# Kernel optimization log

Hardware: AMD Instinct MI355X
Metric: run time of the kernel (lower is better)

The kernel has to match this reference:

```python
import jax, jax.numpy as jnp
import numpy as np


def setup_inputs() -> dict:
    key = jax.random.key(0)
    k1, k2 = jax.random.split(key)
    B = 16384
    y_pred = jax.random.normal(k1, (B,), dtype=jnp.float32)
    y_true = jax.random.randint(k2, (B,), 0, 2, dtype=jnp.int64)
    return {"y_pred": y_pred, "y_true": y_true}


def reference(y_pred, y_true):
    # pos_pred[i] - neg_pred[j] over all (pos, neg) pairs, expressed with a
    # mask-weighted mean so shapes stay static under jit (same math as the
    # boolean-gather version when both classes are present).
    pos = (y_true == 1).astype(y_pred.dtype)  # [B]
    neg = (y_true == 0).astype(y_pred.dtype)  # [B]
    # pairwise_diff[i, j] = y_pred[i] - y_pred[j]
    diff = y_pred[:, None] - y_pred[None, :]  # [B, B]
    w = pos[:, None] * neg[None, :]           # [B, B] pair mask
    s = jax.nn.sigmoid(-diff)
    loss = jnp.sum(s * w) / jnp.sum(w)
    return loss
```

## Files before the change

### kernel.cpp

```cpp
#include <hip/hip_runtime.h>
#include <math.h>


#define NODES 2049
#define NPAD  2052
#define SLEN  4097
#define KC    8
#define HB    8

static constexpr float LO    = -12.0f;
static constexpr float DELTA = 24.0f / 2048.0f;
static constexpr float INVD  = 2048.0f / 24.0f;
static constexpr float LOG2E = 1.4426950408889634f;


__global__ __launch_bounds__(1024)
void hist_k(const float* __restrict__ pred, const int* __restrict__ yt, int B,
            float* __restrict__ g_h ,
            int* __restrict__ g_Pc ) {
    __shared__ __align__(16) float h[2 * NPAD];
    const int t = threadIdx.x;
    const int b = blockIdx.x;

    for (int i = t; i < 2 * NPAD; i += 1024) h[i] = 0.f;
    __syncthreads();

    int cp = 0;
    for (int e = b * 1024 + t; e < B; e += HB * 1024) {
        float p = pred[e];
        int   c = yt[e];
        float x = (p - LO) * INVD;
        x = fminf(fmaxf(x, 0.f), 2047.999f);
        int   k = (int)x;
        float f = x - (float)k;
        int base = (c == 1) ? 0 : NPAD;
        cp += (c == 1);
        atomicAdd(&h[base + k],     1.f - f);
        atomicAdd(&h[base + k + 1], f);
    }
    __syncthreads();

    float* dst = g_h + (size_t)b * 2 * NPAD;
    if (t < 512) {
        ((float4*)dst)[t]          = ((const float4*)h)[t];
        ((float4*)(dst + NPAD))[t] = ((const float4*)(h + NPAD))[t];
    }
    if (t == 0) {
        dst[2048]        = h[2048];
        dst[NPAD + 2048] = h[NPAD + 2048];
    }

    #pragma unroll
    for (int off = 32; off; off >>= 1) cp += __shfl_down(cp, off, 64);
    __shared__ int wc[16];
    if ((t & 63) == 0) wc[t >> 6] = cp;
    __syncthreads();
    if (t == 0) {
        int s = 0;
        #pragma unroll
        for (int k = 0; k < 16; ++k) s += wc[k];
        g_Pc[b] = s;
    }
}


__global__ __launch_bounds__(256)
void conv_k(const float* __restrict__ g_h, float* __restrict__ partial) {
    __shared__ __align__(16) float sS[SLEN];
    __shared__ __align__(16) float sN[NODES];
    const int t = threadIdx.x;
    const int bk = blockIdx.x;

    for (int i = t; i < 512; i += 256) {
        float4 s = make_float4(0.f, 0.f, 0.f, 0.f);
        #pragma unroll
        for (int b = 0; b < HB; ++b) {
            float4 v = ((const float4*)(g_h + (size_t)b * 2 * NPAD + NPAD))[i];
            s.x += v.x; s.y += v.y; s.z += v.z; s.w += v.w;
        }
        ((float4*)sN)[i] = s;
    }
    if (t == 0) {
        float s = 0.f;
        #pragma unroll
        for (int b = 0; b < HB; ++b) s += g_h[(size_t)b * 2 * NPAD + NPAD + 2048];
        sN[2048] = s;
    }
    for (int i = t; i < SLEN; i += 256) {
        float d = (float)(i - 2048) * DELTA;
        float e = __builtin_amdgcn_exp2f(d * LOG2E);
        sS[i] = __builtin_amdgcn_rcpf(1.f + e);
    }
    __syncthreads();

    float acc = 0.f;
    #pragma unroll
    for (int kk = 0; kk < KC; ++kk) {
        int k = bk * KC + kk;
        if (k < NODES) {
            float hPk = 0.f;
            #pragma unroll
            for (int b = 0; b < HB; ++b) hPk += g_h[(size_t)b * 2 * NPAD + k];
            if (hPk != 0.f) {
                const float* Sk = &sS[k + 2048];
                for (int l = t; l < NODES; l += 256)
                    acc += hPk * (sN[l] * Sk[-l]);
            }
        }
    }

    #pragma unroll
    for (int off = 32; off; off >>= 1) acc += __shfl_down(acc, off, 64);
    __shared__ float wa[4];
    if ((t & 63) == 0) wa[t >> 6] = acc;
    __syncthreads();
    if (t == 0) partial[bk] = (wa[0] + wa[1]) + (wa[2] + wa[3]);
}


__global__ __launch_bounds__(256)
void reduce_k(const float* __restrict__ partial, int nPart,
              const int* __restrict__ g_Pc, int B, float* __restrict__ out) {
    const int t = threadIdx.x;
    double s = 0.0;
    for (int i = t; i < nPart; i += 256) s += (double)partial[i];
    int cp = 0;
    if (t < HB) cp = g_Pc[t];
    #pragma unroll
    for (int off = 32; off; off >>= 1) {
        s  += __shfl_down(s, off, 64);
        cp += __shfl_down(cp, off, 64);
    }
    __shared__ double wa[4];
    __shared__ int    wp[4];
    if ((t & 63) == 0) { wa[t >> 6] = s; wp[t >> 6] = cp; }
    __syncthreads();
    if (t == 0) {
        double S = (wa[0] + wa[1]) + (wa[2] + wa[3]);
        double P = (double)(wp[0] + wp[1] + wp[2] + wp[3]);
        double N = (double)B - P;
        out[0] = (float)(S / (P * N));
    }
}

extern "C" void kernel_launch(void* const* d_in, const int* in_sizes, int n_in,
                              void* d_out, int out_size, void* d_ws, size_t ws_size,
                              hipStream_t stream) {
    const float* pred = (const float*)d_in[0];
    const int*   yt   = (const int*)d_in[1];
    const int B = in_sizes[0];
    float* out = (float*)d_out;

    float* g_h  = (float*)d_ws;
    int*   g_Pc = (int*)(g_h + (size_t)HB * 2 * NPAD);
    float* part = (float*)(g_Pc + 64);

    const int nBlk = (NODES + KC - 1) / KC;

    hist_k<<<HB, 1024, 0, stream>>>(pred, yt, B, g_h, g_Pc);
    conv_k<<<nBlk, 256, 0, stream>>>(g_h, part);
    reduce_k<<<1, 256, 0, stream>>>(part, nBlk, g_Pc, B, out);
}
```

Before: 70.99 us.

## Compute only per-block sigmoid window and interchange conv loops for register reuse

Each conv block now computes only the sigmoid values it needs (a window of 2056 entries offset by its node range) instead of the full 4097-entry table, roughly halving the exp/rcp work per block. The loop order is swapped so each thread loads sN[l] once and applies all KC histogram weights held in registers, reusing contiguous table entries. P-histogram weights are gathered before the barrier, overlapping global loads with table setup. The per-k skip for zero weights becomes a single whole-block skip, so blocks with partial zeros do slightly more arithmetic.

```diff
diff --git a/kernel.cpp b/kernel.cpp
--- a/kernel.cpp
+++ b/kernel.cpp
@@ -4,7 +4,7 @@
 
 #define NODES 2049
 #define NPAD  2052
-#define SLEN  4097
+#define TLEN  (2048 + 8)
 #define KC    8
 #define HB    8
 
@@ -66,7 +66,7 @@
 
 __global__ __launch_bounds__(256)
 void conv_k(const float* __restrict__ g_h, float* __restrict__ partial) {
-    __shared__ __align__(16) float sS[SLEN];
+    __shared__ __align__(16) float sT[TLEN];
     __shared__ __align__(16) float sN[NODES];
     const int t = threadIdx.x;
     const int bk = blockIdx.x;
@@ -86,26 +86,35 @@
         for (int b = 0; b < HB; ++b) s += g_h[(size_t)b * 2 * NPAD + NPAD + 2048];
         sN[2048] = s;
     }
-    for (int i = t; i < SLEN; i += 256) {
-        float d = (float)(i - 2048) * DELTA;
+    for (int j = t; j < TLEN; j += 256) {
+        float d = (float)(bk * KC + j - 2048) * DELTA;
         float e = __builtin_amdgcn_exp2f(d * LOG2E);
-        sS[i] = __builtin_amdgcn_rcpf(1.f + e);
+        sT[j] = __builtin_amdgcn_rcpf(1.f + e);
+    }
+
+    float hv[KC];
+    bool anynz = false;
+    #pragma unroll
+    for (int kk = 0; kk < KC; ++kk) {
+        int k = bk * KC + kk;
+        float s = 0.f;
+        if (k < NODES) {
+            #pragma unroll
+            for (int b = 0; b < HB; ++b) s += g_h[(size_t)b * 2 * NPAD + k];
+        }
+        hv[kk] = s;
+        anynz = anynz || (s != 0.f);
     }
     __syncthreads();
 
     float acc = 0.f;
-    #pragma unroll
-    for (int kk = 0; kk < KC; ++kk) {
-        int k = bk * KC + kk;
-        if (k < NODES) {
-            float hPk = 0.f;
+    if (anynz) {
+        for (int l = t; l < NODES; l += 256) {
+            float nv = sN[l];
+            const float* sp = &sT[2048 - l];
             #pragma unroll
-            for (int b = 0; b < HB; ++b) hPk += g_h[(size_t)b * 2 * NPAD + k];
-            if (hPk != 0.f) {
-                const float* Sk = &sS[k + 2048];
-                for (int l = t; l < NODES; l += 256)
-                    acc += hPk * (sN[l] * Sk[-l]);
-            }
+            for (int kk = 0; kk < KC; ++kk)
+                acc += hv[kk] * (nv * sp[kk]);
         }
     }
 
```

After: 68.15 us. -4.0%, faster.
